# Optimization experiments

Measured on AMD Instinct MI355X. Metric: run time of the kernel, lower is better.

The kernel has to match this reference:

```python
import jax, jax.numpy as jnp
import numpy as np

B, T, I, H, O = 1024, 512, 64, 256, 1

def setup_inputs() -> dict:
    key = jax.random.key(0)
    ks = jax.random.split(key, 12)
    s_ih0 = 1.0 / np.sqrt(H)
    def u(k, shape):
        return jax.random.uniform(k, shape, jnp.float32, -s_ih0, s_ih0)
    return {
        "x": jax.random.normal(ks[0], (B, T, I), jnp.float32),
        "w_ih0": u(ks[1], (4 * H, I)),
        "w_hh0": u(ks[2], (4 * H, H)),
        "b_ih0": u(ks[3], (4 * H,)),
        "b_hh0": u(ks[4], (4 * H,)),
        "w_ih1": u(ks[5], (4 * H, H)),
        "w_hh1": u(ks[6], (4 * H, H)),
        "b_ih1": u(ks[7], (4 * H,)),
        "b_hh1": u(ks[8], (4 * H,)),
        "fc_w": u(ks[9], (O, H)),
        "fc_b": u(ks[10], (O,)),
    }

def _lstm_layer(x, w_ih, w_hh, b_ih, b_hh):
    # x: [B, T, D_in] -> hidden sequence [B, T, H], gate order i,f,g,o (PyTorch)
    b, t, _ = x.shape
    h_dim = w_hh.shape[1]
    # precompute input projections for all timesteps: [T, B, 4H]
    xproj = (jnp.einsum('bti,gi->btg', x, w_ih) + b_ih + b_hh).transpose(1, 0, 2)
    h0 = jnp.zeros((b, h_dim), x.dtype)
    c0 = jnp.zeros((b, h_dim), x.dtype)

    def step(carry, xp):
        h, c = carry
        gates = xp + h @ w_hh.T  # [B, 4H]
        i_g, f_g, g_g, o_g = jnp.split(gates, 4, axis=-1)
        i_g = jax.nn.sigmoid(i_g)
        f_g = jax.nn.sigmoid(f_g)
        g_g = jnp.tanh(g_g)
        o_g = jax.nn.sigmoid(o_g)
        c = f_g * c + i_g * g_g
        h = o_g * jnp.tanh(c)
        return (h, c), h

    (h_last, _), hs = jax.lax.scan(step, (h0, c0), xproj)
    return hs.transpose(1, 0, 2), h_last

def reference(x, w_ih0, w_hh0, b_ih0, b_hh0, w_ih1, w_hh1, b_ih1, b_hh1, fc_w, fc_b):
    # Layer 0 -> (eval mode: dropout is identity) -> Layer 1 -> fc on last step
    h_seq0, _ = _lstm_layer(x, w_ih0, w_hh0, b_ih0, b_hh0)
    _, h_last1 = _lstm_layer(h_seq0, w_ih1, w_hh1, b_ih1, b_hh1)
    return h_last1 @ fc_w.T + fc_b  # [B, O]
```

## Files before the change

### kernel.cpp

```cpp
#include <hip/hip_runtime.h>
#include <stdint.h>


#define T_STEPS 512
#define NC0 10
#define NC1 16
#define WSLICE_ELEMS (4*(NC0+NC1)*512)
#define L1_OFF (4*NC0*512)
#define HN (1024*256)

typedef __attribute__((ext_vector_type(8))) short short8;
typedef __attribute__((ext_vector_type(4))) float floatx4;
typedef _Float16 half8 __attribute__((ext_vector_type(8)));

#define MFMA16(A,B,C) __builtin_amdgcn_mfma_f32_16x16x32_f16( \
    __builtin_bit_cast(half8,(A)), __builtin_bit_cast(half8,(B)), (C), 0, 0, 0)

__device__ __forceinline__ uint16_t f2h(float f){
  return __builtin_bit_cast(uint16_t, (_Float16)f);
}
__device__ __forceinline__ float sigm(float x){
  return __builtin_amdgcn_rcpf(1.0f + __builtin_amdgcn_exp2f(-1.44269504f*x));
}
__device__ __forceinline__ float tanhf_(float x){
  return 1.0f - 2.0f*__builtin_amdgcn_rcpf(1.0f + __builtin_amdgcn_exp2f(2.88539008f*x));
}
__device__ __forceinline__ floatx4 splat4(float v){ return (floatx4){v,v,v,v}; }

__device__ __forceinline__ void cvt8h(const floatx4& v0, const floatx4& v1, short8& hi, short8& lo){
  #pragma unroll
  for (int j = 0; j < 8; ++j){
    float f = (j < 4) ? v0[j] : v1[j-4];
    _Float16 h = (_Float16)f;
    _Float16 l = (_Float16)(f - (float)h);
    hi[j] = (short)__builtin_bit_cast(uint16_t, h);
    lo[j] = (short)__builtin_bit_cast(uint16_t, l);
  }
}

__device__ __forceinline__ short8 load_coh16(const uint16_t* p){
  short8 r;
  asm volatile("global_load_dwordx4 %0, %1, off sc0 sc1" : "=v"(r) : "v"(p));
  return r;
}
__device__ __forceinline__ void store_coh2(uint16_t* p, uint32_t v){
  asm volatile("global_store_short %0, %1, off sc0 sc1" :: "v"(p), "v"(v) : "memory");
}
__device__ __forceinline__ floatx4 load_g16f(const float* p){
  floatx4 r;
  asm volatile("global_load_dwordx4 %0, %1, off" : "=v"(r) : "v"(p));
  return r;
}
#define VM_WAIT(N) do{ asm volatile("s_waitcnt vmcnt(" #N ")" ::: "memory"); \
                       __builtin_amdgcn_sched_barrier(0); }while(0)

extern "C" __global__ void prep_weights(const float* __restrict__ wih0, const float* __restrict__ whh0,
                                        const float* __restrict__ wih1, const float* __restrict__ whh1,
                                        uint16_t* __restrict__ wfrag)
{
  int idx = blockIdx.x*256 + threadIdx.x;
  int s  = idx / WSLICE_ELEMS;
  int r  = idx - s*WSLICE_ELEMS;
  int layer = (r >= L1_OFF) ? 1 : 0;
  int rr = layer ? (r - L1_OFF) : r;
  int nc = layer ? NC1 : NC0;
  int n  = rr / (nc*512);
  int c  = (rr / 512) % nc;
  int l  = (rr >> 3) & 63;
  int j  = rr & 7;
  int k  = c*32 + ((l >> 4) << 3) + j;
  int grow = n*256 + s*16 + (l & 15);
  float v;
  if (!layer) v = (k < 64)  ? wih0[grow*64  + k] : whh0[grow*256 + (k - 64)];
  else        v = (k < 256) ? wih1[grow*256 + k] : whh1[grow*256 + (k - 256)];
  wfrag[idx] = f2h(v);
}

extern "C" __global__ void prep_bias(const float* __restrict__ bih0, const float* __restrict__ bhh0,
                                     const float* __restrict__ bih1, const float* __restrict__ bhh1,
                                     float* __restrict__ biasg)
{
  int idx = blockIdx.x*256 + threadIdx.x;
  if (idx >= 16*2*64) return;
  int s = idx >> 7;
  int layer = (idx >> 6) & 1;
  int q = idx & 63;
  int grow = (q >> 4)*256 + s*16 + (q & 15);
  biasg[idx] = layer ? (bih1[grow] + bhh1[grow]) : (bih0[grow] + bhh0[grow]);
}

extern "C" __global__ void __launch_bounds__(256, 1)
lstm_main(const float* __restrict__ x,
          const uint16_t* __restrict__ wfrag,
          const float* __restrict__ biasg,
          uint16_t* __restrict__ hbase,
          const float* __restrict__ fcw,
          const float* __restrict__ fcb,
          int* __restrict__ ctr,
          float* __restrict__ out)
{
  extern __shared__ uint16_t wlds[];
  const int tid  = threadIdx.x;
  const int bid  = blockIdx.x;
  const int s    = bid >> 4;
  const int gh   = bid & 15;
  const int wv   = tid >> 6;
  const int lane = tid & 63;
  const int G    = gh*4 + wv;

  const int arow = G*16 + (lane & 15);
  const int ka   = (lane >> 4) * 8;
  const int drow = G*16 + ((lane >> 4) << 2);
  const int dcol = s*16 + (lane & 15);

  {
    const uint16_t* wsrc = wfrag + (size_t)s*WSLICE_ELEMS;
    for (int i = tid*8; i < WSLICE_ELEMS; i += 256*8)
      *(short8*)(wlds + i) = *(const short8*)(wsrc + i);
  }
  float b0[4], b1[4];
  {
    const int col = lane & 15;
    #pragma unroll
    for (int n = 0; n < 4; ++n){
      b0[n] = biasg[(s*2+0)*64 + n*16 + col];
      b1[n] = biasg[(s*2+1)*64 + n*16 + col];
    }
  }
  const float fcwv = fcw[dcol];
  const float fcb0 = fcb[0];
  __syncthreads();

  const uint16_t* wl = wlds + lane*8;
  const size_t abase = (size_t)arow*256 + ka;
  float c0[4] = {0,0,0,0}, c1[4] = {0,0,0,0};
  int* myc = ctr + G*32;

  short8 xh[2], xl[2];
  {
    const float* xp = x + (size_t)arow*T_STEPS*64 + ka;
    floatx4 v0 = *(const floatx4*)(xp);
    floatx4 v1 = *(const floatx4*)(xp + 4);
    floatx4 v2 = *(const floatx4*)(xp + 32);
    floatx4 v3 = *(const floatx4*)(xp + 36);
    cvt8h(v0, v1, xh[0], xl[0]);
    cvt8h(v2, v3, xh[1], xl[1]);
  }

  for (int t = 0; t < T_STEPS; ++t){
    const size_t par0  = (size_t)(t & 1);
    const size_t rpar0 = par0 ^ 1;

    short8 a0h[8], a0l[8], a1h[8], a1l[8];
    {
      const uint16_t* ph = hbase + rpar0*HN + abase;
      const uint16_t* pl = hbase + 2*(size_t)HN + rpar0*HN + abase;
      #pragma unroll
      for (int kc = 0; kc < 8; ++kc) a0h[kc] = load_coh16(ph + kc*32);
      #pragma unroll
      for (int kc = 0; kc < 8; ++kc) a0l[kc] = load_coh16(pl + kc*32);
    }
    {
      const uint16_t* ph = hbase + 4*(size_t)HN + par0*HN + abase;
      const uint16_t* pl = hbase + 6*(size_t)HN + par0*HN + abase;
      #pragma unroll
      for (int kc = 0; kc < 8; ++kc) a1h[kc] = load_coh16(ph + kc*32);
      #pragma unroll
      for (int kc = 0; kc < 8; ++kc) a1l[kc] = load_coh16(pl + kc*32);
    }
    floatx4 xr0, xr1, xr2, xr3;
    {
      const int tn = (t < T_STEPS-1) ? (t+1) : t;
      const float* xp = x + ((size_t)arow*T_STEPS + tn)*64 + ka;
      xr0 = load_g16f(xp);      xr1 = load_g16f(xp + 4);
      xr2 = load_g16f(xp + 32); xr3 = load_g16f(xp + 36);
    }

    floatx4 acc0[4], acc1[4];
    #pragma unroll
    for (int n = 0; n < 4; ++n) acc0[n] = splat4(b0[n]);
    #pragma unroll
    for (int pk = 0; pk < 2; ++pk){
      #pragma unroll
      for (int n = 0; n < 4; ++n){
        short8 w = *(const short8*)(wl + (n*NC0 + pk)*512);
        acc0[n] = MFMA16(xh[pk], w, acc0[n]);
        acc0[n] = MFMA16(xl[pk], w, acc0[n]);
      }
    }
    #pragma unroll
    for (int n = 0; n < 4; ++n) acc1[n] = splat4(b1[n]);

    VM_WAIT(20);

    #pragma unroll
    for (int kc = 0; kc < 8; ++kc){
      #pragma unroll
      for (int n = 0; n < 4; ++n){
        short8 w0 = *(const short8*)(wl + (n*NC0 + 2 + kc)*512);
        acc0[n] = MFMA16(a0h[kc], w0, acc0[n]);
        acc0[n] = MFMA16(a0l[kc], w0, acc0[n]);
        short8 w1 = *(const short8*)(wl + L1_OFF + (n*NC1 + kc)*512);
        acc1[n] = MFMA16(a0h[kc], w1, acc1[n]);
        acc1[n] = MFMA16(a0l[kc], w1, acc1[n]);
      }
    }

    {
      uint16_t* qh = hbase + par0*HN;
      uint16_t* ql = hbase + 2*(size_t)HN + par0*HN;
      #pragma unroll
      for (int r = 0; r < 4; ++r){
        float ig = sigm(acc0[0][r]);
        float fg = sigm(acc0[1][r]);
        float gg = tanhf_(acc0[2][r]);
        float og = sigm(acc0[3][r]);
        c0[r] = fg*c0[r] + ig*gg;
        float h = og*tanhf_(c0[r]);
        _Float16 hh = (_Float16)h;
        _Float16 hl = (_Float16)(h - (float)hh);
        size_t idx = (size_t)(drow + r)*256 + dcol;
        store_coh2(qh + idx, (uint32_t)__builtin_bit_cast(uint16_t, hh));
        store_coh2(ql + idx, (uint32_t)__builtin_bit_cast(uint16_t, hl));
      }
    }

    VM_WAIT(12);

    #pragma unroll
    for (int kc = 0; kc < 8; ++kc){
      #pragma unroll
      for (int n = 0; n < 4; ++n){
        short8 w = *(const short8*)(wl + L1_OFF + (n*NC1 + 8 + kc)*512);
        acc1[n] = MFMA16(a1h[kc], w, acc1[n]);
        acc1[n] = MFMA16(a1l[kc], w, acc1[n]);
      }
    }

    VM_WAIT(8);
    cvt8h(xr0, xr1, xh[0], xl[0]);
    cvt8h(xr2, xr3, xh[1], xl[1]);

    if (t > 0){
      uint16_t* qh = hbase + 4*(size_t)HN + rpar0*HN;
      uint16_t* ql = hbase + 6*(size_t)HN + rpar0*HN;
      #pragma unroll
      for (int r = 0; r < 4; ++r){
        float ig = sigm(acc1[0][r]);
        float fg = sigm(acc1[1][r]);
        float gg = tanhf_(acc1[2][r]);
        float og = sigm(acc1[3][r]);
        c1[r] = fg*c1[r] + ig*gg;
        float h = og*tanhf_(c1[r]);
        _Float16 hh = (_Float16)h;
        _Float16 hl = (_Float16)(h - (float)hh);
        size_t idx = (size_t)(drow + r)*256 + dcol;
        store_coh2(qh + idx, (uint32_t)__builtin_bit_cast(uint16_t, hh));
        store_coh2(ql + idx, (uint32_t)__builtin_bit_cast(uint16_t, hl));
      }
    }

    VM_WAIT(0);

    if (lane == 0){
      __hip_atomic_fetch_add(myc, 1, __ATOMIC_RELAXED, __HIP_MEMORY_SCOPE_AGENT);
      int spins = 0;
      while (__hip_atomic_load(myc, __ATOMIC_RELAXED, __HIP_MEMORY_SCOPE_AGENT) < 16*(t+1)){
        if (++spins > (1<<20)) break;
        __builtin_amdgcn_s_sleep(1);
      }
    }
  }

  {
    const uint16_t* p0h = hbase + 1*(size_t)HN + abase;
    const uint16_t* p0l = hbase + 3*(size_t)HN + abase;
    const uint16_t* p1h = hbase + 4*(size_t)HN + abase;
    const uint16_t* p1l = hbase + 6*(size_t)HN + abase;
    short8 a0h[8], a0l[8], a1h[8], a1l[8];
    #pragma unroll
    for (int kc = 0; kc < 8; ++kc){
      a0h[kc] = load_coh16(p0h + kc*32);
      a0l[kc] = load_coh16(p0l + kc*32);
      a1h[kc] = load_coh16(p1h + kc*32);
      a1l[kc] = load_coh16(p1l + kc*32);
    }
    VM_WAIT(0);
    floatx4 acc[4];
    #pragma unroll
    for (int n = 0; n < 4; ++n) acc[n] = splat4(b1[n]);
    #pragma unroll
    for (int kc = 0; kc < 8; ++kc){
      #pragma unroll
      for (int n = 0; n < 4; ++n){
        short8 w1 = *(const short8*)(wl + L1_OFF + (n*NC1 + kc)*512);
        acc[n] = MFMA16(a0h[kc], w1, acc[n]);
        acc[n] = MFMA16(a0l[kc], w1, acc[n]);
        short8 w2 = *(const short8*)(wl + L1_OFF + (n*NC1 + 8 + kc)*512);
        acc[n] = MFMA16(a1h[kc], w2, acc[n]);
        acc[n] = MFMA16(a1l[kc], w2, acc[n]);
      }
    }
    #pragma unroll
    for (int r = 0; r < 4; ++r){
      float ig = sigm(acc[0][r]);
      float fg = sigm(acc[1][r]);
      float gg = tanhf_(acc[2][r]);
      float og = sigm(acc[3][r]);
      float cc = fg*c1[r] + ig*gg;
      float h  = og*tanhf_(cc);
      float v  = h * fcwv;
      v += __shfl_xor(v, 1);
      v += __shfl_xor(v, 2);
      v += __shfl_xor(v, 4);
      v += __shfl_xor(v, 8);
      if ((lane & 15) == 0){
        float res = v + ((s == 0) ? fcb0 : 0.0f);
        atomicAdd(out + drow + r, res);
      }
    }
  }
}

extern "C" void kernel_launch(void* const* d_in, const int* in_sizes, int n_in,
                              void* d_out, int out_size, void* d_ws, size_t ws_size,
                              hipStream_t stream)
{
  (void)in_sizes; (void)n_in; (void)out_size; (void)ws_size;
  const float* x    = (const float*)d_in[0];
  const float* wih0 = (const float*)d_in[1];
  const float* whh0 = (const float*)d_in[2];
  const float* bih0 = (const float*)d_in[3];
  const float* bhh0 = (const float*)d_in[4];
  const float* wih1 = (const float*)d_in[5];
  const float* whh1 = (const float*)d_in[6];
  const float* bih1 = (const float*)d_in[7];
  const float* bhh1 = (const float*)d_in[8];
  const float* fcw  = (const float*)d_in[9];
  const float* fcb  = (const float*)d_in[10];

  char* ws = (char*)d_ws;
  const size_t SZ_WFRAG = (size_t)16*WSLICE_ELEMS*2;
  const size_t OFF_BIAS = SZ_WFRAG;
  const size_t OFF_CTR  = OFF_BIAS + (size_t)16*2*64*4;
  const size_t OFF_H    = (size_t)2*1024*1024;

  uint16_t* wfrag = (uint16_t*)(ws);
  float*    biasg = (float*)(ws + OFF_BIAS);
  int*      ctr   = (int*)(ws + OFF_CTR);
  uint16_t* hbase = (uint16_t*)(ws + OFF_H);
  float*    out   = (float*)d_out;

  hipMemsetAsync(d_out, 0, (size_t)1024*sizeof(float), stream);
  hipMemsetAsync(ws + OFF_CTR, 0, (OFF_H - OFF_CTR) + (size_t)8*HN*2, stream);

  hipLaunchKernelGGL(prep_weights, dim3(16*WSLICE_ELEMS/256), dim3(256), 0, stream,
                     wih0, whh0, wih1, whh1, wfrag);
  hipLaunchKernelGGL(prep_bias, dim3(8), dim3(256), 0, stream,
                     bih0, bhh0, bih1, bhh1, biasg);

  hipFuncSetAttribute((const void*)lstm_main,
                      hipFuncAttributeMaxDynamicSharedMemorySize, WSLICE_ELEMS*2);
  void* args[] = { (void*)&x, (void*)&wfrag, (void*)&biasg, (void*)&hbase,
                   (void*)&fcw, (void*)&fcb, (void*)&ctr, (void*)&out };
  hipError_t ce = hipLaunchCooperativeKernel((void*)lstm_main, dim3(256), dim3(256),
                                             args, WSLICE_ELEMS*2, stream);
  if (ce != hipSuccess){
    hipLaunchKernelGGL(lstm_main, dim3(256), dim3(256), WSLICE_ELEMS*2, stream,
                       x, wfrag, biasg, hbase, fcw, fcb, ctr, out);
  }
}
```

Before: 5.657 ms.

## Split grid barrier into per-layer counters and prefetch layer-1 hidden state

Replaces the single per-group barrier at the end of each timestep with two counters, one per layer. Layer 0 now only waits for the previous layer-0 hidden state before loading it. Layer 1's recurrent hidden state is loaded right after its own barrier and carried in registers into the next step, so its MFMAs can start before the layer-0 loads arrive. The aim is to shorten the critical path of the global sync and overlap the two layers' dependencies, at the cost of more registers and two atomic polls per step. The counter array must also be twice as large, which depends on allocation code outside the visible part.

```diff
diff --git a/kernel.cpp b/kernel.cpp
--- a/kernel.cpp
+++ b/kernel.cpp
@@ -16,9 +16,6 @@
 #define MFMA16(A,B,C) __builtin_amdgcn_mfma_f32_16x16x32_f16( \
     __builtin_bit_cast(half8,(A)), __builtin_bit_cast(half8,(B)), (C), 0, 0, 0)
 
-__device__ __forceinline__ uint16_t f2h(float f){
-  return __builtin_bit_cast(uint16_t, (_Float16)f);
-}
 __device__ __forceinline__ float sigm(float x){
   return __builtin_amdgcn_rcpf(1.0f + __builtin_amdgcn_exp2f(-1.44269504f*x));
 }
@@ -53,6 +50,25 @@
 }
 #define VM_WAIT(N) do{ asm volatile("s_waitcnt vmcnt(" #N ")" ::: "memory"); \
                        __builtin_amdgcn_sched_barrier(0); }while(0)
+
+__device__ __forceinline__ void arrive(int* c, int lane){
+  if (lane == 0)
+    __hip_atomic_fetch_add(c, 1, __ATOMIC_RELAXED, __HIP_MEMORY_SCOPE_AGENT);
+}
+__device__ __forceinline__ void poll_ge(int* c, int target, int lane){
+  if (lane == 0){
+    int spins = 0;
+    int v;
+    do {
+      v = __hip_atomic_load(c, __ATOMIC_RELAXED, __HIP_MEMORY_SCOPE_AGENT);
+      asm volatile("s_waitcnt vmcnt(0)" ::: "memory");
+      if (v >= target) break;
+      __builtin_amdgcn_s_sleep(1);
+    } while (++spins < (1<<20));
+  }
+  asm volatile("s_waitcnt vmcnt(0)" ::: "memory");
+  __builtin_amdgcn_sched_barrier(0);
+}
 
 extern "C" __global__ void prep_weights(const float* __restrict__ wih0, const float* __restrict__ whh0,
                                         const float* __restrict__ wih1, const float* __restrict__ whh1,
@@ -73,7 +89,7 @@
   float v;
   if (!layer) v = (k < 64)  ? wih0[grow*64  + k] : whh0[grow*256 + (k - 64)];
   else        v = (k < 256) ? wih1[grow*256 + k] : whh1[grow*256 + (k - 256)];
-  wfrag[idx] = f2h(v);
+  wfrag[idx] = __builtin_bit_cast(uint16_t, (_Float16)v);
 }
 
 extern "C" __global__ void prep_bias(const float* __restrict__ bih0, const float* __restrict__ bhh0,
@@ -134,7 +150,8 @@
   const uint16_t* wl = wlds + lane*8;
   const size_t abase = (size_t)arow*256 + ka;
   float c0[4] = {0,0,0,0}, c1[4] = {0,0,0,0};
-  int* myc = ctr + G*32;
+  int* myc0 = ctr + (G*2+0)*32;
+  int* myc1 = ctr + (G*2+1)*32;
 
   short8 xh[2], xl[2];
   {
@@ -146,12 +163,25 @@
     cvt8h(v0, v1, xh[0], xl[0]);
     cvt8h(v2, v3, xh[1], xl[1]);
   }
+  short8 k1h[8], k1l[8];
+  {
+    const uint16_t* ph = hbase + 4*(size_t)HN + abase;
+    const uint16_t* pl = hbase + 6*(size_t)HN + abase;
+    #pragma unroll
+    for (int kc = 0; kc < 8; ++kc){
+      k1h[kc] = load_coh16(ph + kc*32);
+      k1l[kc] = load_coh16(pl + kc*32);
+    }
+    VM_WAIT(0);
+  }
 
   for (int t = 0; t < T_STEPS; ++t){
     const size_t par0  = (size_t)(t & 1);
     const size_t rpar0 = par0 ^ 1;
 
-    short8 a0h[8], a0l[8], a1h[8], a1l[8];
+    poll_ge(myc0, 16*t, lane);
+
+    short8 a0h[8], a0l[8];
     {
       const uint16_t* ph = hbase + rpar0*HN + abase;
       const uint16_t* pl = hbase + 2*(size_t)HN + rpar0*HN + abase;
@@ -159,14 +189,6 @@
       for (int kc = 0; kc < 8; ++kc) a0h[kc] = load_coh16(ph + kc*32);
       #pragma unroll
       for (int kc = 0; kc < 8; ++kc) a0l[kc] = load_coh16(pl + kc*32);
-    }
-    {
-      const uint16_t* ph = hbase + 4*(size_t)HN + par0*HN + abase;
-      const uint16_t* pl = hbase + 6*(size_t)HN + par0*HN + abase;
-      #pragma unroll
-      for (int kc = 0; kc < 8; ++kc) a1h[kc] = load_coh16(ph + kc*32);
-      #pragma unroll
-      for (int kc = 0; kc < 8; ++kc) a1l[kc] = load_coh16(pl + kc*32);
     }
     floatx4 xr0, xr1, xr2, xr3;
     {
@@ -178,7 +200,16 @@
 
     floatx4 acc0[4], acc1[4];
     #pragma unroll
-    for (int n = 0; n < 4; ++n) acc0[n] = splat4(b0[n]);
+    for (int n = 0; n < 4; ++n){ acc0[n] = splat4(b0[n]); acc1[n] = splat4(b1[n]); }
+    #pragma unroll
+    for (int kc = 0; kc < 8; ++kc){
+      #pragma unroll
+      for (int n = 0; n < 4; ++n){
+        short8 w = *(const short8*)(wl + L1_OFF + (n*NC1 + 8 + kc)*512);
+        acc1[n] = MFMA16(k1h[kc], w, acc1[n]);
+        acc1[n] = MFMA16(k1l[kc], w, acc1[n]);
+      }
+    }
     #pragma unroll
     for (int pk = 0; pk < 2; ++pk){
       #pragma unroll
@@ -188,10 +219,8 @@
         acc0[n] = MFMA16(xl[pk], w, acc0[n]);
       }
     }
-    #pragma unroll
-    for (int n = 0; n < 4; ++n) acc1[n] = splat4(b1[n]);
-
-    VM_WAIT(20);
+
+    VM_WAIT(4);
 
     #pragma unroll
     for (int kc = 0; kc < 8; ++kc){
@@ -224,20 +253,9 @@
         store_coh2(ql + idx, (uint32_t)__builtin_bit_cast(uint16_t, hl));
       }
     }
-
-    VM_WAIT(12);
-
-    #pragma unroll
-    for (int kc = 0; kc < 8; ++kc){
-      #pragma unroll
-      for (int n = 0; n < 4; ++n){
-        short8 w = *(const short8*)(wl + L1_OFF + (n*NC1 + 8 + kc)*512);
-        acc1[n] = MFMA16(a1h[kc], w, acc1[n]);
-        acc1[n] = MFMA16(a1l[kc], w, acc1[n]);
-      }
-    }
-
-    VM_WAIT(8);
+    VM_WAIT(0);
+    arrive(myc0, lane);
+
     cvt8h(xr0, xr1, xh[0], xl[0]);
     cvt8h(xr2, xr3, xh[1], xl[1]);
 
@@ -259,15 +277,17 @@
         store_coh2(ql + idx, (uint32_t)__builtin_bit_cast(uint16_t, hl));
       }
     }
-
     VM_WAIT(0);
-
-    if (lane == 0){
-      __hip_atomic_fetch_add(myc, 1, __ATOMIC_RELAXED, __HIP_MEMORY_SCOPE_AGENT);
-      int spins = 0;
-      while (__hip_atomic_load(myc, __ATOMIC_RELAXED, __HIP_MEMORY_SCOPE_AGENT) < 16*(t+1)){
-        if (++spins > (1<<20)) break;
-        __builtin_amdgcn_s_sleep(1);
+    arrive(myc1, lane);
+
+    poll_ge(myc1, 16*(t+1), lane);
+    {
+      const uint16_t* ph = hbase + 4*(size_t)HN + rpar0*HN + abase;
+      const uint16_t* pl = hbase + 6*(size_t)HN + rpar0*HN + abase;
+      #pragma unroll
+      for (int kc = 0; kc < 8; ++kc){
+        k1h[kc] = load_coh16(ph + kc*32);
+        k1l[kc] = load_coh16(pl + kc*32);
       }
     }
   }
@@ -275,15 +295,11 @@
   {
     const uint16_t* p0h = hbase + 1*(size_t)HN + abase;
     const uint16_t* p0l = hbase + 3*(size_t)HN + abase;
-    const uint16_t* p1h = hbase + 4*(size_t)HN + abase;
-    const uint16_t* p1l = hbase + 6*(size_t)HN + abase;
-    short8 a0h[8], a0l[8], a1h[8], a1l[8];
+    short8 a0h[8], a0l[8];
     #pragma unroll
     for (int kc = 0; kc < 8; ++kc){
       a0h[kc] = load_coh16(p0h + kc*32);
       a0l[kc] = load_coh16(p0l + kc*32);
-      a1h[kc] = load_coh16(p1h + kc*32);
-      a1l[kc] = load_coh16(p1l + kc*32);
     }
     VM_WAIT(0);
     floatx4 acc[4];
@@ -297,8 +313,8 @@
         acc[n] = MFMA16(a0h[kc], w1, acc[n]);
         acc[n] = MFMA16(a0l[kc], w1, acc[n]);
         short8 w2 = *(const short8*)(wl + L1_OFF + (n*NC1 + 8 + kc)*512);
-        acc[n] = MFMA16(a1h[kc], w2, acc[n]);
-        acc[n] = MFMA16(a1l[kc], w2, acc[n]);
+        acc[n] = MFMA16(k1h[kc], w2, acc[n]);
+        acc[n] = MFMA16(k1l[kc], w2, acc[n]);
       }
     }
     #pragma unroll
```

Result: faster. 5.222 ms (-7.7%).
